# Kernel optimization log

Measured on AMD Instinct MI355X. Metric: run time of the kernel, lower is better.

## Reference

```python
import jax, jax.numpy as jnp
import numpy as np

EPS = 1e-5

def conv3x3(x, w, bias=None):
    y = jax.lax.conv_general_dilated(x, w, (1, 1), 'SAME',
                                     dimension_numbers=('NCHW', 'OIHW', 'NCHW'))
    if bias is not None:
        y = y + bias[None, :, None, None]
    return y

def batchnorm(x, g, b):
    m = x.mean((0, 2, 3), keepdims=True)
    v = x.var((0, 2, 3), keepdims=True)
    return (x - m) * jax.lax.rsqrt(v + EPS) * g[None, :, None, None] + b[None, :, None, None]

def deform_sample(x, offset, mask, dg=2):
    # x: [B,C,H,W]; offset: [B,dg*9*2,H,W] (dy,dx interleaved per mmcv); mask: [B,dg*9,H,W]
    B, C, H, W = x.shape
    K = 9
    cg = C // dg
    off = offset.reshape(B, dg, K, 2, H, W)
    dy, dx = off[:, :, :, 0], off[:, :, :, 1]
    m = mask.reshape(B, dg, K, H, W)
    ky = (jnp.repeat(jnp.arange(3), 3) - 1).astype(x.dtype)   # kernel row offset per tap
    kx = (jnp.tile(jnp.arange(3), 3) - 1).astype(x.dtype)     # kernel col offset per tap
    py = dy + jnp.arange(H, dtype=x.dtype)[None, None, None, :, None] + ky[None, None, :, None, None]
    px = dx + jnp.arange(W, dtype=x.dtype)[None, None, None, None, :] + kx[None, None, :, None, None]
    y0 = jnp.floor(py); x0 = jnp.floor(px)
    ly = py - y0; lx = px - x0
    y0i = y0.astype(jnp.int32); x0i = x0.astype(jnp.int32)
    y1i = y0i + 1; x1i = x0i + 1
    def ok(yy, xx):
        return ((yy >= 0) & (yy < H) & (xx >= 0) & (xx < W)).astype(x.dtype)
    xg = x.reshape(B, dg, cg, H * W)
    def gather(yy, xx):
        idx = (jnp.clip(yy, 0, H - 1) * W + jnp.clip(xx, 0, W - 1)).reshape(B, dg, -1)
        g = jax.vmap(jax.vmap(lambda im, ii: im[:, ii]))(xg, idx)   # [B,dg,cg,K*H*W]
        return g.reshape(B, dg, cg, K, H, W)
    w00 = ((1 - ly) * (1 - lx) * ok(y0i, x0i))[:, :, None]
    w01 = ((1 - ly) * lx * ok(y0i, x1i))[:, :, None]
    w10 = (ly * (1 - lx) * ok(y1i, x0i))[:, :, None]
    w11 = (ly * lx * ok(y1i, x1i))[:, :, None]
    val = (gather(y0i, x0i) * w00 + gather(y0i, x1i) * w01 +
           gather(y1i, x0i) * w10 + gather(y1i, x1i) * w11)
    return val * m[:, :, None]   # [B,dg,cg,K,H,W]

def reference(input_v, input_i, off_w, off_b, dconv_w, bn1_g, bn1_b, conv2_w, bn2_g, bn2_b):
    x = jnp.concatenate([input_v, input_i], axis=1)             # [B,C,H,W]
    off_all = conv3x3(x, off_w, off_b)                          # [B,54,H,W]
    o1, o2, mask = jnp.split(off_all, 3, axis=1)
    offset = jnp.concatenate([o1, o2], axis=1)                  # [B,36,H,W]
    mask = jax.nn.sigmoid(mask)                                 # [B,18,H,W]
    sampled = deform_sample(x, offset, mask, dg=2)              # [B,2,cg,9,H,W]
    O = dconv_w.shape[0]
    out = jnp.einsum('bgckhw,ogck->bohw', sampled, dconv_w.reshape(O, 2, -1, 9))
    out = jax.nn.relu(batchnorm(out, bn1_g, bn1_b))
    out = jax.nn.relu(batchnorm(conv3x3(out, conv2_w), bn2_g, bn2_b))
    return out

def setup_inputs() -> dict:
    key = jax.random.key(0)
    ks = jax.random.split(key, 8)
    B, Cm, O, H, W = 4, 128, 128, 64, 64
    C = 2 * Cm
    inp = {}
    inp['input_v'] = jax.random.normal(ks[0], (B, Cm, H, W), jnp.float32)
    inp['input_i'] = jax.random.normal(ks[1], (B, Cm, H, W), jnp.float32)
    # offset/mask conv (zero-init in torch; small random here for a non-trivial reference)
    inp['off_w'] = jax.random.normal(ks[2], (54, C, 3, 3), jnp.float32) * 0.02
    inp['off_b'] = jnp.zeros((54,), jnp.float32)
    inp['dconv_w'] = jax.random.normal(ks[3], (O, C, 3, 3), jnp.float32) * (1.0 / np.sqrt(C * 9))
    inp['bn1_g'] = jnp.ones((O,), jnp.float32)
    inp['bn1_b'] = jnp.zeros((O,), jnp.float32)
    inp['conv2_w'] = jax.random.normal(ks[4], (O, O, 3, 3), jnp.float32) * (1.0 / np.sqrt(O * 9))
    inp['bn2_g'] = jnp.ones((O,), jnp.float32)
    inp['bn2_b'] = jnp.zeros((O,), jnp.float32)
    return inp
```

## Files before the change

### kernel.cpp

```cpp
#include <hip/hip_runtime.h>

#define EPSBN 1e-5f

using s8v = __attribute__((ext_vector_type(8))) short;
using f4v = __attribute__((ext_vector_type(4))) float;

__device__ inline unsigned short f2bf(float f) {
  unsigned u = __float_as_uint(f);
  return (unsigned short)((u + 0x7FFFu + ((u >> 16) & 1u)) >> 16);
}
__device__ inline float bf2f(unsigned short h) {
  return __uint_as_float(((unsigned)h) << 16);
}

__global__ __launch_bounds__(256) void k_pack(const float* __restrict__ v, const float* __restrict__ im,
                                              unsigned short* __restrict__ xb) {
  __shared__ float tile[64][33];
  int b = blockIdx.z;
  int hw0 = blockIdx.x * 32;
  int c0 = blockIdx.y * 64;
  int tx = threadIdx.x, ty = threadIdx.y;
#pragma unroll
  for (int i = 0; i < 64; i += 8) {
    int c = c0 + ty + i;
    const float* src = (c < 128) ? (v + ((size_t)b * 128 + c) * 4096)
                                 : (im + ((size_t)b * 128 + (c - 128)) * 4096);
    tile[ty + i][tx] = src[hw0 + tx];
  }
  __syncthreads();
#pragma unroll
  for (int i = 0; i < 32; i += 8) {
    int hw = hw0 + ty + i;
    ushort2 o;
    o.x = f2bf(tile[2 * tx][ty + i]);
    o.y = f2bf(tile[2 * tx + 1][ty + i]);
    *(ushort2*)&xb[((size_t)(b * 4096 + hw)) * 256 + c0 + 2 * tx] = o;
  }
}

__global__ __launch_bounds__(256) void k_wprep_off(const float* __restrict__ w, unsigned short* __restrict__ wt) {
  int id = blockIdx.x * 256 + threadIdx.x;
  int lane = id & 63;
  int nb = (id >> 6) & 3;
  int ks = id >> 8;
  int ks2 = ks & 1, tap = (ks >> 1) % 9, cc = ks / 18;
  int o = nb * 16 + (lane & 15);
  int cb = cc * 64 + ks2 * 32 + ((lane >> 4) * 8);
  s8v r;
#pragma unroll
  for (int j = 0; j < 8; ++j) {
    float val = (o < 54) ? w[((size_t)o * 256 + cb + j) * 9 + tap] : 0.f;
    r[j] = (short)f2bf(val);
  }
  *(s8v*)&wt[(size_t)id * 8] = r;
}
__global__ __launch_bounds__(256) void k_wprep_d(const float* __restrict__ w, unsigned short* __restrict__ wt) {
  int id = blockIdx.x * 256 + threadIdx.x;
  int lane = id & 63;
  int nb = (id >> 6) & 7;
  int kstep = id >> 9;
  int chunk = kstep >> 2, ks4 = kstep & 3;
  int g = chunk / 9, kk = chunk % 9;
  int o = nb * 16 + (lane & 15);
  int cb = g * 128 + ks4 * 32 + ((lane >> 4) * 8);
  s8v r;
#pragma unroll
  for (int j = 0; j < 8; ++j) r[j] = (short)f2bf(w[((size_t)o * 256 + cb + j) * 9 + kk]);
  *(s8v*)&wt[(size_t)id * 8] = r;
}
__global__ __launch_bounds__(256) void k_wprep_2(const float* __restrict__ w, unsigned short* __restrict__ wt) {
  int id = blockIdx.x * 256 + threadIdx.x;
  int lane = id & 63;
  int nb = (id >> 6) & 7;
  int kstep = id >> 9;
  int ks2 = kstep & 1, tap = (kstep >> 1) % 9, cc = kstep / 18;
  int o = nb * 16 + (lane & 15);
  int cb = cc * 64 + ks2 * 32 + ((lane >> 4) * 8);
  s8v r;
#pragma unroll
  for (int j = 0; j < 8; ++j) r[j] = (short)f2bf(w[((size_t)o * 128 + cb + j) * 9 + tap]);
  *(s8v*)&wt[(size_t)id * 8] = r;
}

__global__ __launch_bounds__(512, 3) void k_offconv(const unsigned short* __restrict__ xb,
                                                    const unsigned short* __restrict__ wt,
                                                    const float* __restrict__ bias,
                                                    float* __restrict__ off) {
  __shared__ char Xs[102 * 512];
  __shared__ float redx[2048];
  int bid = blockIdx.x;
  int id8 = (bid & 7) * 64 + (bid >> 3);
  int w0 = (id8 & 1) * 32;
  int h = (id8 >> 1) & 63;
  int b = id8 >> 7;
  int t = threadIdx.x;
  int l = t & 63, wv = t >> 6;
  int og = wv & 3, kh = wv >> 2;
  f4v zero = {0.f, 0.f, 0.f, 0.f};
  f4v acc[2] = {zero, zero};

  for (int id = t; id < 3264; id += 512) {
    int tr = id >> 5, oq8 = id & 31;
    int ky = tr / 34, col = tr % 34;
    int hh = h + ky - 1, ww = w0 + col - 1;
    s8v val = {0, 0, 0, 0, 0, 0, 0, 0};
    if ((unsigned)hh < 64u && (unsigned)ww < 64u)
      val = *(const s8v*)&xb[(((size_t)(b * 64 + hh)) * 64 + ww) * 256 + oq8 * 8];
    int byte = (tr * 512 + oq8 * 16) ^ ((tr & 7) << 4);
    *(s8v*)(Xs + byte) = val;
  }
  __syncthreads();
  int khi = l >> 4, lo = l & 15;
#pragma unroll
  for (int tap = 0; tap < 9; ++tap) {
    int ky = tap / 3, kx = tap % 3;
#pragma unroll
    for (int s = 0; s < 4; ++s) {
      int cc = kh * 2 + (s >> 1);
      int ks2 = s & 1;
      int kstep = cc * 18 + tap * 2 + ks2;
      int chb = cc * 128 + ks2 * 64 + khi * 16;
      s8v bfr = *(const s8v*)&wt[((size_t)(kstep * 4 + og) * 64 + l) * 8];
#pragma unroll
      for (int m = 0; m < 2; ++m) {
        int tr = ky * 34 + m * 16 + lo + kx;
        int rbyte = (tr * 512 + chb) ^ ((tr & 7) << 4);
        s8v a = *(const s8v*)(Xs + rbyte);
        acc[m] = __builtin_amdgcn_mfma_f32_16x16x32_bf16(a, bfr, acc[m], 0, 0, 0);
      }
    }
  }
  if (kh == 1) {
#pragma unroll
    for (int m = 0; m < 2; ++m)
#pragma unroll
      for (int j = 0; j < 4; ++j) redx[((og * 64 + l) * 2 + m) * 4 + j] = acc[m][j];
  }
  __syncthreads();
  if (kh == 0) {
    int o = og * 16 + lo;
    int pixb = (b * 64 + h) * 64 + w0;
    if (o < 54) {
      float bi = bias[o];
#pragma unroll
      for (int m = 0; m < 2; ++m)
#pragma unroll
        for (int j = 0; j < 4; ++j) {
          int px = pixb + m * 16 + khi * 4 + j;
          float vv = acc[m][j] + redx[((og * 64 + l) * 2 + m) * 4 + j] + bi;
          if (o >= 36) vv = 1.f / (1.f + __expf(-vv));
          off[(size_t)px * 54 + o] = vv;
        }
    }
  }
}

#define DC_ISSUE(c, V, Q)                                   \
  do {                                                      \
    const unsigned* ip_ = sidx[(c)][px];                    \
    const float* qp_ = swt[(c)][px];                        \
    Q##0 = qp_[0]; Q##1 = qp_[1]; Q##2 = qp_[2]; Q##3 = qp_[3]; \
    V##0 = *(const s8v*)&xb[ip_[0] + chof];                 \
    V##1 = *(const s8v*)&xb[ip_[1] + chof];                 \
    V##2 = *(const s8v*)&xb[ip_[2] + chof];                 \
    V##3 = *(const s8v*)&xb[ip_[3] + chof];                 \
  } while (0)

#define DC_COMMIT(c, V, Q)                                  \
  do {                                                      \
    unsigned rr_[4];                                        \
    _Pragma("unroll") for (int jp_ = 0; jp_ < 4; ++jp_) {   \
      float f0_ = Q##0 * bf2f((unsigned short)V##0[2 * jp_]) +     \
                  Q##1 * bf2f((unsigned short)V##1[2 * jp_]) +     \
                  Q##2 * bf2f((unsigned short)V##2[2 * jp_]) +     \
                  Q##3 * bf2f((unsigned short)V##3[2 * jp_]);      \
      float f1_ = Q##0 * bf2f((unsigned short)V##0[2 * jp_ + 1]) + \
                  Q##1 * bf2f((unsigned short)V##1[2 * jp_ + 1]) + \
                  Q##2 * bf2f((unsigned short)V##2[2 * jp_ + 1]) + \
                  Q##3 * bf2f((unsigned short)V##3[2 * jp_ + 1]);  \
      unsigned p_;                                          \
      asm("v_cvt_pk_bf16_f32 %0, %1, %2" : "=v"(p_) : "v"(f0_), "v"(f1_)); \
      rr_[jp_] = p_;                                        \
    }                                                       \
    *(int4*)(&At[(c) & 1][0] + wbyte) = *(int4*)rr_;        \
  } while (0)

#define LDS_BARRIER()                                        \
  do {                                                       \
    asm volatile("s_waitcnt lgkmcnt(0)" ::: "memory");       \
    __builtin_amdgcn_s_barrier();                            \
  } while (0)

__global__ __launch_bounds__(512, 3) void k_dconv(const unsigned short* __restrict__ xb,
                                                  const float* __restrict__ off,
                                                  const unsigned short* __restrict__ wt,
                                                  float* __restrict__ y1p,
                                                  float* __restrict__ st1, float* __restrict__ st2) {
  __shared__ unsigned int sidx[18][32][4];
  __shared__ float swt[18][32][4];
  __shared__ char At[2][8192];
  int t = threadIdx.x;
  int l = t & 63, og = t >> 6;
  int bid = blockIdx.x;
  int id8 = (bid & 7) * 64 + (bid >> 3);
  int pixb = id8 * 32;
  int b = pixb >> 12, h = (pixb >> 6) & 63, w0 = pixb & 63;

  for (int id = t; id < 576; id += 512) {
    int chunk = id >> 5, ppx = id & 31;
    int g = chunk / 9, kk = chunk % 9;
    const float* op = off + (size_t)(pixb + ppx) * 54;
    float dy = op[(g * 9 + kk) * 2];
    float dx = op[(g * 9 + kk) * 2 + 1];
    float msk = op[36 + g * 9 + kk];
    float py = dy + (float)(h + kk / 3 - 1);
    float pxf = dx + (float)(w0 + ppx + kk % 3 - 1);
    float y0f = floorf(py), x0f = floorf(pxf);
    float ly = py - y0f, lx = pxf - x0f;
    int y0 = (int)y0f, x0 = (int)x0f;
    int y1 = y0 + 1, x1 = x0 + 1;
    float oky0 = (y0 >= 0 && y0 < 64) ? 1.f : 0.f;
    float oky1 = (y1 >= 0 && y1 < 64) ? 1.f : 0.f;
    float okx0 = (x0 >= 0 && x0 < 64) ? 1.f : 0.f;
    float okx1 = (x1 >= 0 && x1 < 64) ? 1.f : 0.f;
    int y0c = min(max(y0, 0), 63), y1c = min(max(y1, 0), 63);
    int x0c = min(max(x0, 0), 63), x1c = min(max(x1, 0), 63);
    unsigned base = (unsigned)(b * 4096);
    unsigned gofs = (unsigned)(g * 128);
    sidx[chunk][ppx][0] = (base + y0c * 64 + x0c) * 256u + gofs;
    sidx[chunk][ppx][1] = (base + y0c * 64 + x1c) * 256u + gofs;
    sidx[chunk][ppx][2] = (base + y1c * 64 + x0c) * 256u + gofs;
    sidx[chunk][ppx][3] = (base + y1c * 64 + x1c) * 256u + gofs;
    swt[chunk][ppx][0] = (1.f - ly) * (1.f - lx) * oky0 * okx0 * msk;
    swt[chunk][ppx][1] = (1.f - ly) * lx * oky0 * okx1 * msk;
    swt[chunk][ppx][2] = ly * (1.f - lx) * oky1 * okx0 * msk;
    swt[chunk][ppx][3] = ly * lx * oky1 * okx1 * msk;
  }
  __syncthreads();

  int px = t >> 4, oq = t & 15;
  unsigned chof = oq * 8u;
  int wbyte = (px * 256 + oq * 16) ^ ((px & 7) << 4);
  int khi = l >> 4, lo = l & 15;

  s8v va0, va1, va2, va3, vb0, vb1, vb2, vb3;
  float qa0, qa1, qa2, qa3, qb0, qb1, qb2, qb3;

  DC_ISSUE(0, va, qa);
  DC_ISSUE(1, vb, qb);
  DC_COMMIT(0, va, qa);
  LDS_BARRIER();

  f4v zero = {0.f, 0.f, 0.f, 0.f};
  f4v acc[2] = {zero, zero};

  for (int c = 0; c < 18; ++c) {
    if (c < 16) {
      if ((c & 1) == 0) DC_ISSUE(c + 2, va, qa);
      else              DC_ISSUE(c + 2, vb, qb);
    }
#pragma unroll
    for (int ks4 = 0; ks4 < 4; ++ks4) {
      int kstep = c * 4 + ks4;
      s8v bfr = *(const s8v*)&wt[((size_t)(kstep * 8 + og) * 64 + l) * 8];
      int chb = ks4 * 64 + khi * 16;
#pragma unroll
      for (int m = 0; m < 2; ++m) {
        int trA = m * 16 + lo;
        int rbyte = (trA * 256 + chb) ^ ((trA & 7) << 4);
        s8v a = *(const s8v*)(&At[c & 1][0] + rbyte);
        acc[m] = __builtin_amdgcn_mfma_f32_16x16x32_bf16(a, bfr, acc[m], 0, 0, 0);
      }
    }
    if (c < 17) {
      if ((c & 1) == 0) DC_COMMIT(c + 1, vb, qb);
      else              DC_COMMIT(c + 1, va, qa);
    }
    LDS_BARRIER();
  }

  int o = og * 16 + lo;
  float s1v = 0.f, s2v = 0.f;
#pragma unroll
  for (int m = 0; m < 2; ++m)
#pragma unroll
    for (int j = 0; j < 4; ++j) {
      float vv = acc[m][j];
      y1p[(size_t)(pixb + m * 16 + khi * 4 + j) * 128 + o] = vv;
      s1v += vv; s2v += vv * vv;
    }
  float* red = &swt[0][0][0];
  red[khi * 128 + o] = s1v;
  red[512 + khi * 128 + o] = s2v;
  __syncthreads();
  if (t < 128) {
    float a1 = 0.f, a2 = 0.f;
#pragma unroll
    for (int rr = 0; rr < 4; ++rr) { a1 += red[rr * 128 + t]; a2 += red[512 + rr * 128 + t]; }
    atomicAdd(&st1[t], a1);
    atomicAdd(&st2[t], a2);
  }
}

__global__ __launch_bounds__(256) void k_bnrelu1(const float* __restrict__ yp, const float* __restrict__ s1,
                                                 const float* __restrict__ s2, const float* __restrict__ g,
                                                 const float* __restrict__ bb, unsigned short* __restrict__ yb) {
  __shared__ float sc[128], sh[128];
  int t = threadIdx.x;
  if (t < 128) {
    float m = s1[t] * (1.f / 16384.f);
    float var = s2[t] * (1.f / 16384.f) - m * m;
    float s = g[t] * rsqrtf(var + EPSBN);
    sc[t] = s;
    sh[t] = bb[t] - m * s;
  }
  __syncthreads();
  size_t i = ((size_t)blockIdx.x * 256 + t) * 8;
  int c0 = (int)(i & 127);
  float4 u = *(const float4*)&yp[i];
  float4 v = *(const float4*)&yp[i + 4];
  s8v r;
  r[0] = (short)f2bf(fmaxf(0.f, u.x * sc[c0 + 0] + sh[c0 + 0]));
  r[1] = (short)f2bf(fmaxf(0.f, u.y * sc[c0 + 1] + sh[c0 + 1]));
  r[2] = (short)f2bf(fmaxf(0.f, u.z * sc[c0 + 2] + sh[c0 + 2]));
  r[3] = (short)f2bf(fmaxf(0.f, u.w * sc[c0 + 3] + sh[c0 + 3]));
  r[4] = (short)f2bf(fmaxf(0.f, v.x * sc[c0 + 4] + sh[c0 + 4]));
  r[5] = (short)f2bf(fmaxf(0.f, v.y * sc[c0 + 5] + sh[c0 + 5]));
  r[6] = (short)f2bf(fmaxf(0.f, v.z * sc[c0 + 6] + sh[c0 + 6]));
  r[7] = (short)f2bf(fmaxf(0.f, v.w * sc[c0 + 7] + sh[c0 + 7]));
  *(s8v*)&yb[i] = r;
}

__global__ __launch_bounds__(512, 3) void k_conv2(const unsigned short* __restrict__ yb,
                                                  const unsigned short* __restrict__ wt,
                                                  float* __restrict__ y2p,
                                                  float* __restrict__ st1, float* __restrict__ st2) {
  __shared__ char Bs[102 * 256];
  int bid = blockIdx.x;
  int id8 = (bid & 7) * 64 + (bid >> 3);
  int w0 = (id8 & 1) * 32;
  int h = (id8 >> 1) & 63;
  int b = id8 >> 7;
  int t = threadIdx.x;
  int l = t & 63, og = t >> 6;
  f4v zero = {0.f, 0.f, 0.f, 0.f};
  f4v acc[2] = {zero, zero};

  for (int id = t; id < 1632; id += 512) {
    int tr = id >> 4, oq = id & 15;
    int ky = tr / 34, col = tr % 34;
    int hh = h + ky - 1, ww = w0 + col - 1;
    s8v val = {0, 0, 0, 0, 0, 0, 0, 0};
    if ((unsigned)hh < 64u && (unsigned)ww < 64u)
      val = *(const s8v*)&yb[(((size_t)(b * 64 + hh)) * 64 + ww) * 128 + oq * 8];
    int byte = (tr * 256 + oq * 16) ^ ((tr & 7) << 4);
    *(s8v*)(Bs + byte) = val;
  }
  __syncthreads();
  int khi = l >> 4, lo = l & 15;
#pragma unroll
  for (int tap = 0; tap < 9; ++tap) {
    int ky = tap / 3, kx = tap % 3;
#pragma unroll
    for (int ks4 = 0; ks4 < 4; ++ks4) {
      int kstep = ((ks4 >> 1) * 9 + tap) * 2 + (ks4 & 1);
      s8v bfr = *(const s8v*)&wt[((size_t)(kstep * 8 + og) * 64 + l) * 8];
      int chb = ks4 * 64 + khi * 16;
#pragma unroll
      for (int m = 0; m < 2; ++m) {
        int tr = ky * 34 + m * 16 + lo + kx;
        int rbyte = (tr * 256 + chb) ^ ((tr & 7) << 4);
        s8v a = *(const s8v*)(Bs + rbyte);
        acc[m] = __builtin_amdgcn_mfma_f32_16x16x32_bf16(a, bfr, acc[m], 0, 0, 0);
      }
    }
  }
  __syncthreads();
  int pixb = (b * 64 + h) * 64 + w0;
  int o = og * 16 + lo;
  float s1v = 0.f, s2v = 0.f;
#pragma unroll
  for (int m = 0; m < 2; ++m)
#pragma unroll
    for (int j = 0; j < 4; ++j) {
      float vv = acc[m][j];
      y2p[(size_t)(pixb + m * 16 + khi * 4 + j) * 128 + o] = vv;
      s1v += vv; s2v += vv * vv;
    }
  float* red = (float*)Bs;
  red[khi * 128 + o] = s1v;
  red[512 + khi * 128 + o] = s2v;
  __syncthreads();
  if (t < 128) {
    float a1 = 0.f, a2 = 0.f;
#pragma unroll
    for (int rr = 0; rr < 4; ++rr) { a1 += red[rr * 128 + t]; a2 += red[512 + rr * 128 + t]; }
    atomicAdd(&st1[t], a1);
    atomicAdd(&st2[t], a2);
  }
}

__global__ __launch_bounds__(256) void k_bnrelu2(const float* __restrict__ yp, const float* __restrict__ s1,
                                                 const float* __restrict__ s2, const float* __restrict__ g,
                                                 const float* __restrict__ bb, float* __restrict__ out) {
  __shared__ float sc[128], sh[128];
  int t = threadIdx.x;
  if (t < 128) {
    float m = s1[t] * (1.f / 16384.f);
    float var = s2[t] * (1.f / 16384.f) - m * m;
    float s = g[t] * rsqrtf(var + EPSBN);
    sc[t] = s;
    sh[t] = bb[t] - m * s;
  }
  __syncthreads();
  int bh = blockIdx.x;
  int b = bh >> 6, h = bh & 63;
  const float* src = yp + (size_t)bh * 64 * 128;
  for (int id = t; id < 64 * 128; id += 256) {
    int w = id & 63, o = id >> 6;
    float v = src[w * 128 + o];
    v = fmaxf(0.f, v * sc[o] + sh[o]);
    out[(((size_t)b * 128 + o) * 64 + h) * 64 + w] = v;
  }
}

extern "C" void kernel_launch(void* const* d_in, const int* in_sizes, int n_in,
                              void* d_out, int out_size, void* d_ws, size_t ws_size,
                              hipStream_t stream) {
  const float* in_v = (const float*)d_in[0];
  const float* in_i = (const float*)d_in[1];
  const float* off_w = (const float*)d_in[2];
  const float* off_b = (const float*)d_in[3];
  const float* dconv_w = (const float*)d_in[4];
  const float* bn1_g = (const float*)d_in[5];
  const float* bn1_b = (const float*)d_in[6];
  const float* conv2_w = (const float*)d_in[7];
  const float* bn2_g = (const float*)d_in[8];
  const float* bn2_b = (const float*)d_in[9];
  float* out = (float*)d_out;

  char* w = (char*)d_ws;
  unsigned short* xb = (unsigned short*)w;      w += (size_t)16384 * 256 * 2;
  float* off_nhwc = (float*)w;                  w += (size_t)16384 * 54 * 4;
  unsigned short* wtf_off = (unsigned short*)w; w += (size_t)18432 * 8 * 2;
  unsigned short* wtf_d = (unsigned short*)w;   w += (size_t)36864 * 8 * 2;
  unsigned short* wtf_2 = (unsigned short*)w;   w += (size_t)18432 * 8 * 2;
  float* y1p = (float*)w;                       w += (size_t)16384 * 128 * 4;
  unsigned short* y1b = (unsigned short*)w;     w += (size_t)16384 * 128 * 2;
  float* y2p = (float*)w;                       w += (size_t)16384 * 128 * 4;
  float* stats = (float*)w;                     w += 512 * 4;

  hipMemsetAsync(stats, 0, 512 * 4, stream);
  k_pack<<<dim3(128, 4, 4), dim3(32, 8), 0, stream>>>(in_v, in_i, xb);
  k_wprep_off<<<72, 256, 0, stream>>>(off_w, wtf_off);
  k_wprep_d<<<144, 256, 0, stream>>>(dconv_w, wtf_d);
  k_wprep_2<<<72, 256, 0, stream>>>(conv2_w, wtf_2);
  k_offconv<<<512, 512, 0, stream>>>(xb, wtf_off, off_b, off_nhwc);
  k_dconv<<<512, 512, 0, stream>>>(xb, off_nhwc, wtf_d, y1p, stats, stats + 128);
  k_bnrelu1<<<1024, 256, 0, stream>>>(y1p, stats, stats + 128, bn1_g, bn1_b, y1b);
  k_conv2<<<512, 512, 0, stream>>>(y1b, wtf_2, y2p, stats + 256, stats + 384);
  k_bnrelu2<<<256, 256, 0, stream>>>(y2p, stats + 256, stats + 384, bn2_g, bn2_b, out);
}
```

Measured before the change: 171.0 us.

## Widen dconv tile to full rows, merge weight prep, LDS-transpose bnrelu2

The deformable conv kernel now handles 64 pixels (a full image row) per block instead of 32, with each thread gathering 16 channels rather than 8. This doubles the per-wave MFMA accumulators and halves the grid to 256 blocks, and launch bounds drop to 2 waves-groups per CU to fit the larger LDS and register footprint. The bilinear blend now unpacks bf16 pairs with shift and mask operations on 32-bit words. The three weight-prep kernels are merged into one launch to cut launch overhead, and bnrelu2 stages its tile through padded shared memory with float4 loads so the NHWC-to-NCHW transpose reads coalesced, at the risk of lower occupancy and fewer blocks than CUs in dconv.

```diff
diff --git a/kernel.cpp b/kernel.cpp
--- a/kernel.cpp
+++ b/kernel.cpp
@@ -8,9 +8,6 @@
 __device__ inline unsigned short f2bf(float f) {
   unsigned u = __float_as_uint(f);
   return (unsigned short)((u + 0x7FFFu + ((u >> 16) & 1u)) >> 16);
-}
-__device__ inline float bf2f(unsigned short h) {
-  return __uint_as_float(((unsigned)h) << 16);
 }
 
 __global__ __launch_bounds__(256) void k_pack(const float* __restrict__ v, const float* __restrict__ im,
@@ -38,48 +35,54 @@
   }
 }
 
-__global__ __launch_bounds__(256) void k_wprep_off(const float* __restrict__ w, unsigned short* __restrict__ wt) {
-  int id = blockIdx.x * 256 + threadIdx.x;
-  int lane = id & 63;
-  int nb = (id >> 6) & 3;
-  int ks = id >> 8;
-  int ks2 = ks & 1, tap = (ks >> 1) % 9, cc = ks / 18;
-  int o = nb * 16 + (lane & 15);
-  int cb = cc * 64 + ks2 * 32 + ((lane >> 4) * 8);
-  s8v r;
-#pragma unroll
-  for (int j = 0; j < 8; ++j) {
-    float val = (o < 54) ? w[((size_t)o * 256 + cb + j) * 9 + tap] : 0.f;
-    r[j] = (short)f2bf(val);
-  }
-  *(s8v*)&wt[(size_t)id * 8] = r;
-}
-__global__ __launch_bounds__(256) void k_wprep_d(const float* __restrict__ w, unsigned short* __restrict__ wt) {
-  int id = blockIdx.x * 256 + threadIdx.x;
-  int lane = id & 63;
-  int nb = (id >> 6) & 7;
-  int kstep = id >> 9;
-  int chunk = kstep >> 2, ks4 = kstep & 3;
-  int g = chunk / 9, kk = chunk % 9;
-  int o = nb * 16 + (lane & 15);
-  int cb = g * 128 + ks4 * 32 + ((lane >> 4) * 8);
-  s8v r;
-#pragma unroll
-  for (int j = 0; j < 8; ++j) r[j] = (short)f2bf(w[((size_t)o * 256 + cb + j) * 9 + kk]);
-  *(s8v*)&wt[(size_t)id * 8] = r;
-}
-__global__ __launch_bounds__(256) void k_wprep_2(const float* __restrict__ w, unsigned short* __restrict__ wt) {
-  int id = blockIdx.x * 256 + threadIdx.x;
-  int lane = id & 63;
-  int nb = (id >> 6) & 7;
-  int kstep = id >> 9;
-  int ks2 = kstep & 1, tap = (kstep >> 1) % 9, cc = kstep / 18;
-  int o = nb * 16 + (lane & 15);
-  int cb = cc * 64 + ks2 * 32 + ((lane >> 4) * 8);
-  s8v r;
-#pragma unroll
-  for (int j = 0; j < 8; ++j) r[j] = (short)f2bf(w[((size_t)o * 128 + cb + j) * 9 + tap]);
-  *(s8v*)&wt[(size_t)id * 8] = r;
+__global__ __launch_bounds__(256) void k_wprep_all(const float* __restrict__ w_off,
+                                                   const float* __restrict__ w_d,
+                                                   const float* __restrict__ w_2,
+                                                   unsigned short* __restrict__ wt_off,
+                                                   unsigned short* __restrict__ wt_d,
+                                                   unsigned short* __restrict__ wt_2) {
+  int bid = blockIdx.x, t = threadIdx.x;
+  if (bid < 72) {
+    int id = bid * 256 + t;
+    int lane = id & 63;
+    int nb = (id >> 6) & 3;
+    int ks = id >> 8;
+    int ks2 = ks & 1, tap = (ks >> 1) % 9, cc = ks / 18;
+    int o = nb * 16 + (lane & 15);
+    int cb = cc * 64 + ks2 * 32 + ((lane >> 4) * 8);
+    s8v r;
+#pragma unroll
+    for (int j = 0; j < 8; ++j) {
+      float val = (o < 54) ? w_off[((size_t)o * 256 + cb + j) * 9 + tap] : 0.f;
+      r[j] = (short)f2bf(val);
+    }
+    *(s8v*)&wt_off[(size_t)id * 8] = r;
+  } else if (bid < 216) {
+    int id = (bid - 72) * 256 + t;
+    int lane = id & 63;
+    int nb = (id >> 6) & 7;
+    int kstep = id >> 9;
+    int chunk = kstep >> 2, ks4 = kstep & 3;
+    int g = chunk / 9, kk = chunk % 9;
+    int o = nb * 16 + (lane & 15);
+    int cb = g * 128 + ks4 * 32 + ((lane >> 4) * 8);
+    s8v r;
+#pragma unroll
+    for (int j = 0; j < 8; ++j) r[j] = (short)f2bf(w_d[((size_t)o * 256 + cb + j) * 9 + kk]);
+    *(s8v*)&wt_d[(size_t)id * 8] = r;
+  } else {
+    int id = (bid - 216) * 256 + t;
+    int lane = id & 63;
+    int nb = (id >> 6) & 7;
+    int kstep = id >> 9;
+    int ks2 = kstep & 1, tap = (kstep >> 1) % 9, cc = kstep / 18;
+    int o = nb * 16 + (lane & 15);
+    int cb = cc * 64 + ks2 * 32 + ((lane >> 4) * 8);
+    s8v r;
+#pragma unroll
+    for (int j = 0; j < 8; ++j) r[j] = (short)f2bf(w_2[((size_t)o * 128 + cb + j) * 9 + tap]);
+    *(s8v*)&wt_2[(size_t)id * 8] = r;
+  }
 }
 
 __global__ __launch_bounds__(512, 3) void k_offconv(const unsigned short* __restrict__ xb,
@@ -160,29 +163,39 @@
     const unsigned* ip_ = sidx[(c)][px];                    \
     const float* qp_ = swt[(c)][px];                        \
     Q##0 = qp_[0]; Q##1 = qp_[1]; Q##2 = qp_[2]; Q##3 = qp_[3]; \
-    V##0 = *(const s8v*)&xb[ip_[0] + chof];                 \
-    V##1 = *(const s8v*)&xb[ip_[1] + chof];                 \
-    V##2 = *(const s8v*)&xb[ip_[2] + chof];                 \
-    V##3 = *(const s8v*)&xb[ip_[3] + chof];                 \
+    V##00 = *(const s8v*)&xb[ip_[0] + chof0];               \
+    V##01 = *(const s8v*)&xb[ip_[1] + chof0];               \
+    V##02 = *(const s8v*)&xb[ip_[2] + chof0];               \
+    V##03 = *(const s8v*)&xb[ip_[3] + chof0];               \
+    V##10 = *(const s8v*)&xb[ip_[0] + chof1];               \
+    V##11 = *(const s8v*)&xb[ip_[1] + chof1];               \
+    V##12 = *(const s8v*)&xb[ip_[2] + chof1];               \
+    V##13 = *(const s8v*)&xb[ip_[3] + chof1];               \
+  } while (0)
+
+#define DC_HALF(c, A0, A1, A2, A3, Q, WB)                               \
+  do {                                                                  \
+    unsigned rr_[4];                                                    \
+    _Pragma("unroll") for (int jp_ = 0; jp_ < 4; ++jp_) {               \
+      unsigned w0_ = ((const unsigned*)&A0)[jp_];                       \
+      unsigned w1_ = ((const unsigned*)&A1)[jp_];                       \
+      unsigned w2_ = ((const unsigned*)&A2)[jp_];                       \
+      unsigned w3_ = ((const unsigned*)&A3)[jp_];                       \
+      float e_ = Q##0 * __uint_as_float(w0_ << 16) + Q##1 * __uint_as_float(w1_ << 16) + \
+                 Q##2 * __uint_as_float(w2_ << 16) + Q##3 * __uint_as_float(w3_ << 16);  \
+      float o_ = Q##0 * __uint_as_float(w0_ & 0xffff0000u) + Q##1 * __uint_as_float(w1_ & 0xffff0000u) + \
+                 Q##2 * __uint_as_float(w2_ & 0xffff0000u) + Q##3 * __uint_as_float(w3_ & 0xffff0000u);  \
+      unsigned p_;                                                      \
+      asm("v_cvt_pk_bf16_f32 %0, %1, %2" : "=v"(p_) : "v"(e_), "v"(o_)); \
+      rr_[jp_] = p_;                                                    \
+    }                                                                   \
+    *(int4*)(&At[(c) & 1][0] + (WB)) = *(int4*)rr_;                     \
   } while (0)
 
 #define DC_COMMIT(c, V, Q)                                  \
   do {                                                      \
-    unsigned rr_[4];                                        \
-    _Pragma("unroll") for (int jp_ = 0; jp_ < 4; ++jp_) {   \
-      float f0_ = Q##0 * bf2f((unsigned short)V##0[2 * jp_]) +     \
-                  Q##1 * bf2f((unsigned short)V##1[2 * jp_]) +     \
-                  Q##2 * bf2f((unsigned short)V##2[2 * jp_]) +     \
-                  Q##3 * bf2f((unsigned short)V##3[2 * jp_]);      \
-      float f1_ = Q##0 * bf2f((unsigned short)V##0[2 * jp_ + 1]) + \
-                  Q##1 * bf2f((unsigned short)V##1[2 * jp_ + 1]) + \
-                  Q##2 * bf2f((unsigned short)V##2[2 * jp_ + 1]) + \
-                  Q##3 * bf2f((unsigned short)V##3[2 * jp_ + 1]);  \
-      unsigned p_;                                          \
-      asm("v_cvt_pk_bf16_f32 %0, %1, %2" : "=v"(p_) : "v"(f0_), "v"(f1_)); \
-      rr_[jp_] = p_;                                        \
-    }                                                       \
-    *(int4*)(&At[(c) & 1][0] + wbyte) = *(int4*)rr_;        \
+    DC_HALF(c, V##00, V##01, V##02, V##03, Q, wbyte0);      \
+    DC_HALF(c, V##10, V##11, V##12, V##13, Q, wbyte1);      \
   } while (0)
 
 #define LDS_BARRIER()                                        \
@@ -191,30 +204,30 @@
     __builtin_amdgcn_s_barrier();                            \
   } while (0)
 
-__global__ __launch_bounds__(512, 3) void k_dconv(const unsigned short* __restrict__ xb,
+__global__ __launch_bounds__(512, 2) void k_dconv(const unsigned short* __restrict__ xb,
                                                   const float* __restrict__ off,
                                                   const unsigned short* __restrict__ wt,
                                                   float* __restrict__ y1p,
                                                   float* __restrict__ st1, float* __restrict__ st2) {
-  __shared__ unsigned int sidx[18][32][4];
-  __shared__ float swt[18][32][4];
-  __shared__ char At[2][8192];
+  __shared__ unsigned int sidx[18][64][4];
+  __shared__ float swt[18][64][4];
+  __shared__ char At[2][16384];
   int t = threadIdx.x;
   int l = t & 63, og = t >> 6;
   int bid = blockIdx.x;
-  int id8 = (bid & 7) * 64 + (bid >> 3);
-  int pixb = id8 * 32;
-  int b = pixb >> 12, h = (pixb >> 6) & 63, w0 = pixb & 63;
-
-  for (int id = t; id < 576; id += 512) {
-    int chunk = id >> 5, ppx = id & 31;
+  int id8 = (bid & 7) * 32 + (bid >> 3);
+  int pixb = id8 * 64;
+  int b = id8 >> 6, h = id8 & 63;
+
+  for (int id = t; id < 1152; id += 512) {
+    int chunk = id >> 6, ppx = id & 63;
     int g = chunk / 9, kk = chunk % 9;
     const float* op = off + (size_t)(pixb + ppx) * 54;
     float dy = op[(g * 9 + kk) * 2];
     float dx = op[(g * 9 + kk) * 2 + 1];
     float msk = op[36 + g * 9 + kk];
     float py = dy + (float)(h + kk / 3 - 1);
-    float pxf = dx + (float)(w0 + ppx + kk % 3 - 1);
+    float pxf = dx + (float)(ppx + kk % 3 - 1);
     float y0f = floorf(py), x0f = floorf(pxf);
     float ly = py - y0f, lx = pxf - x0f;
     int y0 = (int)y0f, x0 = (int)x0f;
@@ -238,12 +251,15 @@
   }
   __syncthreads();
 
-  int px = t >> 4, oq = t & 15;
-  unsigned chof = oq * 8u;
-  int wbyte = (px * 256 + oq * 16) ^ ((px & 7) << 4);
+  int px = t >> 3;
+  int cq = t & 7;
+  unsigned chof0 = cq * 16u, chof1 = cq * 16u + 8u;
+  int wbyte0 = (px * 256 + cq * 32) ^ ((px & 7) << 4);
+  int wbyte1 = (px * 256 + cq * 32 + 16) ^ ((px & 7) << 4);
   int khi = l >> 4, lo = l & 15;
 
-  s8v va0, va1, va2, va3, vb0, vb1, vb2, vb3;
+  s8v va00, va01, va02, va03, va10, va11, va12, va13;
+  s8v vb00, vb01, vb02, vb03, vb10, vb11, vb12, vb13;
   float qa0, qa1, qa2, qa3, qb0, qb1, qb2, qb3;
 
   DC_ISSUE(0, va, qa);
@@ -252,7 +268,7 @@
   LDS_BARRIER();
 
   f4v zero = {0.f, 0.f, 0.f, 0.f};
-  f4v acc[2] = {zero, zero};
+  f4v acc[4] = {zero, zero, zero, zero};
 
   for (int c = 0; c < 18; ++c) {
     if (c < 16) {
@@ -265,7 +281,7 @@
       s8v bfr = *(const s8v*)&wt[((size_t)(kstep * 8 + og) * 64 + l) * 8];
       int chb = ks4 * 64 + khi * 16;
 #pragma unroll
-      for (int m = 0; m < 2; ++m) {
+      for (int m = 0; m < 4; ++m) {
         int trA = m * 16 + lo;
         int rbyte = (trA * 256 + chb) ^ ((trA & 7) << 4);
         s8v a = *(const s8v*)(&At[c & 1][0] + rbyte);
@@ -282,7 +298,7 @@
   int o = og * 16 + lo;
   float s1v = 0.f, s2v = 0.f;
 #pragma unroll
-  for (int m = 0; m < 2; ++m)
+  for (int m = 0; m < 4; ++m)
 #pragma unroll
     for (int j = 0; j < 4; ++j) {
       float vv = acc[m][j];
@@ -404,6 +420,7 @@
                                                  const float* __restrict__ s2, const float* __restrict__ g,
                                                  const float* __restrict__ bb, float* __restrict__ out) {
   __shared__ float sc[128], sh[128];
+  __shared__ float buf[64 * 129];
   int t = threadIdx.x;
   if (t < 128) {
     float m = s1[t] * (1.f / 16384.f);
@@ -412,13 +429,19 @@
     sc[t] = s;
     sh[t] = bb[t] - m * s;
   }
-  __syncthreads();
   int bh = blockIdx.x;
   int b = bh >> 6, h = bh & 63;
-  const float* src = yp + (size_t)bh * 64 * 128;
-  for (int id = t; id < 64 * 128; id += 256) {
-    int w = id & 63, o = id >> 6;
-    float v = src[w * 128 + o];
+  const float* src = yp + (size_t)bh * 8192;
+  for (int i = t; i < 2048; i += 256) {
+    float4 v = ((const float4*)src)[i];
+    int w = (i * 4) >> 7, o = (i * 4) & 127;
+    float* d = &buf[w * 129 + o];
+    d[0] = v.x; d[1] = v.y; d[2] = v.z; d[3] = v.w;
+  }
+  __syncthreads();
+  for (int id = t; id < 8192; id += 256) {
+    int o = id >> 6, w = id & 63;
+    float v = buf[w * 129 + o];
     v = fmaxf(0.f, v * sc[o] + sh[o]);
     out[(((size_t)b * 128 + o) * 64 + h) * 64 + w] = v;
   }
@@ -452,11 +475,9 @@
 
   hipMemsetAsync(stats, 0, 512 * 4, stream);
   k_pack<<<dim3(128, 4, 4), dim3(32, 8), 0, stream>>>(in_v, in_i, xb);
-  k_wprep_off<<<72, 256, 0, stream>>>(off_w, wtf_off);
-  k_wprep_d<<<144, 256, 0, stream>>>(dconv_w, wtf_d);
-  k_wprep_2<<<72, 256, 0, stream>>>(conv2_w, wtf_2);
+  k_wprep_all<<<288, 256, 0, stream>>>(off_w, dconv_w, conv2_w, wtf_off, wtf_d, wtf_2);
   k_offconv<<<512, 512, 0, stream>>>(xb, wtf_off, off_b, off_nhwc);
-  k_dconv<<<512, 512, 0, stream>>>(xb, off_nhwc, wtf_d, y1p, stats, stats + 128);
+  k_dconv<<<256, 512, 0, stream>>>(xb, off_nhwc, wtf_d, y1p, stats, stats + 128);
   k_bnrelu1<<<1024, 256, 0, stream>>>(y1p, stats, stats + 128, bn1_g, bn1_b, y1b);
   k_conv2<<<512, 512, 0, stream>>>(y1b, wtf_2, y2p, stats + 256, stats + 384);
   k_bnrelu2<<<256, 256, 0, stream>>>(y2p, stats + 256, stats + 384, bn2_g, bn2_b, out);
```

After: 176.3 us. 3.1% more time.
